# Kernel optimization log

Measured on AMD Instinct MI355X. Metric: run time of the kernel, lower is better.

The kernel has to match this reference:

```python
import jax, jax.numpy as jnp
import numpy as np
import itertools

# ---- constants matching init_kwargs ----
ED, KD, NH, AR = 512, 16, 8, 4
D = AR * KD            # 64 == ED // NH (required by cascade residual add)
DH = D * NH            # 512
RES, WS = 28, 7
SCALE = KD ** -0.5
KS = [7, 5, 3, 3, 3, 3, 3, 3]

# relative-position bias index map for a WSxWS window (49 unique |offset| pairs)
def _bias_idx(ws):
    pts = list(itertools.product(range(ws), range(ws)))
    offs, idxs = {}, []
    for p1 in pts:
        for p2 in pts:
            o = (abs(p1[0] - p2[0]), abs(p1[1] - p2[1]))
            if o not in offs:
                offs[o] = len(offs)
            idxs.append(offs[o])
    return np.array(idxs, dtype=np.int32).reshape(ws * ws, ws * ws), len(offs)
BIAS_IDX, N_OFFS = _bias_idx(WS)  # [49,49], 49


def dwconv(x, w, b):
    """Depthwise conv, stride 1, SAME padding (pad = k//2, odd k). w: [C,1,k,k]."""
    y = jax.lax.conv_general_dilated(x, w, (1, 1), 'SAME',
                                     dimension_numbers=('NCHW', 'OIHW', 'NCHW'),
                                     feature_group_count=x.shape[1])
    return y + b[None, :, None, None]


def pw(x, w, b):
    """1x1 conv (fused Conv2d_BN in eval mode). w: [O,C]."""
    return jnp.einsum('bchw,oc->bohw', x, w) + b[None, :, None, None]


def mlp(x, w1, b1, w2, b2):
    return pw(jax.nn.hard_swish(pw(x, w1, b1)), w2, b2)


def window_partition(x, ws):
    B, C, H, W = x.shape
    nH, nW = H // ws, W // ws
    return x.reshape(B, C, nH, ws, nW, ws).transpose(0, 2, 4, 1, 3, 5).reshape(B * nH * nW, C, ws, ws)


def window_merge(xw, B, H, W, ws):
    nH, nW = H // ws, W // ws
    C = xw.shape[1]
    return xw.reshape(B, nH, nW, C, ws, ws).transpose(0, 3, 1, 4, 2, 5).reshape(B, C, H, W)


def cascade_attention(xw, qkv_w, qkv_b, dwq_ws, dwq_bs, ab, proj_w, proj_b):
    """xw: [Bw, ED, WS, WS]; ab: [NH, N, N] bias table gathered per head."""
    Bw, C, H, W = xw.shape
    N = H * W
    spx = jnp.split(xw, NH, axis=1)          # NH chunks of [Bw, ED//NH, H, W]
    sp = spx[0]
    outs = []
    for i in range(NH):  # heads are structurally distinct (kernel sizes) -> Python loop ok
        if i > 0:
            sp = sp + spx[i]
        y = pw(sp, qkv_w[i], qkv_b[i])       # [Bw, 2*KD+D, H, W]
        q, k, v = jnp.split(y, [KD, 2 * KD], axis=1)
        q = dwconv(q, dwq_ws[i], dwq_bs[i])  # per-head depthwise conv on q
        qf = q.reshape(Bw, KD, N)
        kf = k.reshape(Bw, KD, N)
        vf = v.reshape(Bw, D, N)
        attn = jnp.einsum('bcn,bcm->bnm', qf, kf) * SCALE + ab[i]
        attn = jax.nn.softmax(attn, axis=-1)
        sp = jnp.einsum('bdm,bnm->bdn', vf, attn).reshape(Bw, D, H, W)
        outs.append(sp)
    y = jnp.concatenate(outs, axis=1)        # [Bw, DH, H, W]
    y = jax.nn.hard_swish(y)                 # proj = Sequential(act, Conv2d_BN)
    return pw(y, proj_w, proj_b)


def _forward(x, dw0_w, dw0_b, ffn0_w1, ffn0_b1, ffn0_w2, ffn0_b2,
             qkv_w, qkv_b, dwq_w7, dwq_b7, dwq_w5, dwq_b5, dwq_w3, dwq_b3,
             attn_bias, proj_w, proj_b,
             dw1_w, dw1_b, ffn1_w1, ffn1_b1, ffn1_w2, ffn1_b2):
    B, C, H, W = x.shape
    dwq_ws = [dwq_w7, dwq_w5] + [dwq_w3[i] for i in range(6)]
    dwq_bs = [dwq_b7, dwq_b5] + [dwq_b3[i] for i in range(6)]
    ab = attn_bias[:, BIAS_IDX]              # [NH, 49, 49]
    x = x + dwconv(x, dw0_w, dw0_b)
    x = x + mlp(x, ffn0_w1, ffn0_b1, ffn0_w2, ffn0_b2)
    xw = window_partition(x, WS)
    aw = cascade_attention(xw, qkv_w, qkv_b, dwq_ws, dwq_bs, ab, proj_w, proj_b)
    x = x + window_merge(aw, B, H, W, WS)
    x = x + dwconv(x, dw1_w, dw1_b)
    x = x + mlp(x, ffn1_w1, ffn1_b1, ffn1_w2, ffn1_b2)
    return x


def setup_inputs() -> dict:
    key = jax.random.key(0)
    ks = jax.random.split(key, 24)
    B = 64
    r = lambda k, shape, s=0.05: (jax.random.normal(k, shape, dtype=jnp.float32) * s)
    qkv_out = 2 * KD + D  # 96
    inp = {
        'x': jax.random.normal(ks[0], (B, ED, RES, RES), dtype=jnp.float32),
        'dw0_w': r(ks[1], (ED, 1, 3, 3)), 'dw0_b': r(ks[2], (ED,)),
        'ffn0_w1': r(ks[3], (2 * ED, ED)), 'ffn0_b1': r(ks[4], (2 * ED,)),
        'ffn0_w2': r(ks[5], (ED, 2 * ED)), 'ffn0_b2': r(ks[6], (ED,)),
        'qkv_w': r(ks[7], (NH, qkv_out, ED // NH)), 'qkv_b': r(ks[8], (NH, qkv_out)),
        'dwq_w7': r(ks[9], (KD, 1, 7, 7)), 'dwq_b7': r(ks[10], (KD,)),
        'dwq_w5': r(ks[11], (KD, 1, 5, 5)), 'dwq_b5': r(ks[12], (KD,)),
        'dwq_w3': r(ks[13], (6, KD, 1, 3, 3)), 'dwq_b3': r(ks[14], (6, KD)),
        'attn_bias': r(ks[15], (NH, N_OFFS)),
        'proj_w': r(ks[16], (ED, DH)), 'proj_b': r(ks[17], (ED,)),
        'dw1_w': r(ks[18], (ED, 1, 3, 3)), 'dw1_b': r(ks[19], (ED,)),
        'ffn1_w1': r(ks[20], (2 * ED, ED)), 'ffn1_b1': r(ks[21], (2 * ED,)),
        'ffn1_w2': r(ks[22], (ED, 2 * ED)), 'ffn1_b2': r(ks[23], (ED,)),
    }
    return inp


def reference(x, dw0_w, dw0_b, ffn0_w1, ffn0_b1, ffn0_w2, ffn0_b2,
              qkv_w, qkv_b, dwq_w7, dwq_b7, dwq_w5, dwq_b5, dwq_w3, dwq_b3,
              attn_bias, proj_w, proj_b,
              dw1_w, dw1_b, ffn1_w1, ffn1_b1, ffn1_w2, ffn1_b2):
    return _forward(x, dw0_w, dw0_b, ffn0_w1, ffn0_b1, ffn0_w2, ffn0_b2,
                    qkv_w, qkv_b, dwq_w7, dwq_b7, dwq_w5, dwq_b5, dwq_w3, dwq_b3,
                    attn_bias, proj_w, proj_b,
                    dw1_w, dw1_b, ffn1_w1, ffn1_b1, ffn1_w2, ffn1_b2)
```

## Files before the change

### kernel.cpp

```cpp
#include <hip/hip_runtime.h>
#include <hip/hip_bf16.h>


#define NPOS 50176
#define NEL ((size_t)512 * NPOS)

typedef __hip_bfloat16 hbf;
typedef unsigned int u32;
typedef __attribute__((ext_vector_type(8))) short short8;
typedef __attribute__((ext_vector_type(4))) short bf16x4;
typedef __attribute__((ext_vector_type(4))) float f32x4;

__device__ __forceinline__ float hswish(float v) {
    float t = fminf(fmaxf(v + 3.0f, 0.0f), 6.0f);
    return v * t * (1.0f / 6.0f);
}
__device__ __forceinline__ float b2f(hbf x) { return __bfloat162float(x); }
__device__ __forceinline__ hbf f2b(float x) { return __float2bfloat16(x); }

__device__ __forceinline__ unsigned short bfb(float v) {
    hbf h = f2b(v); unsigned short u; __builtin_memcpy(&u, &h, 2); return u;
}
__device__ __forceinline__ unsigned pk2(float a, float b) {
    return (unsigned)bfb(a) | ((unsigned)bfb(b) << 16);
}
__device__ __forceinline__ int swz128(int row, int b) {
    return row * 128 + (b ^ ((row & 7) << 4));
}
__device__ __forceinline__ void gl16(const hbf* g, short* l) {
    __builtin_amdgcn_global_load_lds((const __attribute__((address_space(1))) u32*)g,
                                     (__attribute__((address_space(3))) u32*)l,
                                     16, 0, 0);
}

__device__ __forceinline__ bool is_bf16_buf(const void* probe) {
    const unsigned* w = (const unsigned*)probe;
    int hits = 0;
#pragma unroll
    for (int i = 0; i < 64; i++) {
        unsigned lo = w[i] & 0xFFFFu;
        unsigned e = (lo >> 7) & 0xFFu;
        hits += ((e >= 100u && e <= 140u) || lo == 0u) ? 1 : 0;
    }
    return hits >= 32;
}

#define OFF_W01  0
#define OFF_W02  524288
#define OFF_W11  1048576
#define OFF_W12  1572864
#define OFF_PW   2097152
#define OFF_QKVW 2359296
#define OFF_QKVB 2408448
#define OFF_W7   2409216
#define OFF_B7   2410000
#define OFF_W5   2410016
#define OFF_B5   2410416
#define OFF_W3   2410432
#define OFF_B3   2411296
#define OFF_AB   2411392
#define OFF_D0W  2411784
#define OFF_D0B  2416392
#define OFF_D1W  2416904
#define OFF_D1B  2421512
#define OFF_B01  2422024
#define OFF_B02  2423048
#define OFF_B11  2423560
#define OFF_B12  2424584
#define OFF_PB   2425096
#define ARENA_TOT 2425608

struct CvtArgs { const void* src; int off; int count; };
struct CvtTable { CvtArgs t[23]; };

__global__ __launch_bounds__(256) void k_convert(CvtTable tab, hbf* __restrict__ arena,
                                                 const void* __restrict__ probe) {
    CvtArgs a = tab.t[blockIdx.y];
    int i = blockIdx.x * 256 + threadIdx.x;
    if (i >= a.count) return;
    bool isbf = is_bf16_buf(probe);
    float v = isbf ? b2f(((const hbf*)a.src)[i]) : ((const float*)a.src)[i];
    arena[a.off + i] = f2b(v);
}

template <int EPI, int K, int GX, bool SWAP>
__global__ __launch_bounds__(256) void k_gemm(const hbf* __restrict__ A,
                                              const hbf* __restrict__ B,
                                              const hbf* __restrict__ bias,
                                              const void* __restrict__ res,
                                              void* __restrict__ out,
                                              const void* __restrict__ probe) {
    __shared__ short sA[128 * 64];
    __shared__ short sB[128 * 64];

    const int tid = threadIdx.x;
    const int wave = tid >> 6, lane = tid & 63;
    const int col = lane & 15, quad = lane >> 4;

    const int lin = blockIdx.y * GX + blockIdx.x;
    const int q8 = (GX * (int)gridDim.y) >> 3;
    const int swz = (lin & 7) * q8 + (lin >> 3);
    const int bx = swz % GX, by = swz / GX;
    const int m0 = (SWAP ? by : bx) * 128, n0 = (SWAP ? bx : by) * 128;

    const int wm = (wave & 1) * 64, wn = (wave >> 1) * 64;

    const int rowl = lane >> 3;
    const int kswz = ((lane & 7) ^ rowl) * 8;
    const hbf* Ag = A + (size_t)(m0 + wave * 32 + rowl) * K + kswz;
    const hbf* Bg = B + (size_t)(n0 + wave * 32 + rowl) * K + kswz;
    short* sAw = sA + (wave * 32) * 64;
    short* sBw = sB + (wave * 32) * 64;

    f32x4 acc[4][4];
#pragma unroll
    for (int i = 0; i < 4; i++)
#pragma unroll
        for (int j = 0; j < 4; j++) acc[i][j] = (f32x4){0.f, 0.f, 0.f, 0.f};

    for (int k0 = 0; k0 < K; k0 += 64) {
        __syncthreads();
#pragma unroll
        for (int t = 0; t < 4; t++) {
            gl16(Ag + k0 + (size_t)t * 8 * K, sAw + t * 8 * 64);
            gl16(Bg + k0 + (size_t)t * 8 * K, sBw + t * 8 * 64);
        }
        __syncthreads();

#pragma unroll
        for (int kk = 0; kk < 2; kk++) {
            short8 af[4], bfr[4];
#pragma unroll
            for (int i = 0; i < 4; i++) {
                int r = wm + i * 16 + col;
                af[i] = *(const short8*)(sA + r * 64 + (((kk * 4 + quad) ^ (r & 7)) * 8));
            }
#pragma unroll
            for (int j = 0; j < 4; j++) {
                int r = wn + j * 16 + col;
                bfr[j] = *(const short8*)(sB + r * 64 + (((kk * 4 + quad) ^ (r & 7)) * 8));
            }
#pragma unroll
            for (int i = 0; i < 4; i++)
#pragma unroll
                for (int j = 0; j < 4; j++)
                    acc[i][j] = __builtin_amdgcn_mfma_f32_16x16x32_bf16(af[i], bfr[j], acc[i][j], 0, 0, 0);
        }
    }

    bool outbf = false;
    if constexpr (EPI == 3) outbf = is_bf16_buf(probe);

#pragma unroll
    for (int i = 0; i < 4; i++) {
#pragma unroll
        for (int j = 0; j < 4; j++) {
#pragma unroll
            for (int r = 0; r < 4; r++) {
                int mi = m0 + wm + i * 16 + quad * 4 + r;
                int nj = n0 + wn + j * 16 + col;
                float v = acc[i][j][r];
                if constexpr (EPI == 0) {
                    v = hswish(v + b2f(bias[nj]));
                    ((hbf*)out)[(size_t)mi * 1024 + nj] = f2b(v);
                } else if constexpr (EPI == 1) {
                    v += b2f(bias[mi]) + b2f(((const hbf*)res)[(size_t)nj * 512 + mi]);
                    ((float*)out)[(size_t)mi * NPOS + nj] = v;
                } else if constexpr (EPI == 2) {
                    int w = nj / 49, p = nj % 49;
                    int nct = (w >> 4) * 784 + (((w >> 2) & 3) * 7 + p / 7) * 28 + (w & 3) * 7 + p % 7;
                    size_t oi = (size_t)mi * NPOS + nct;
                    v += b2f(bias[mi]) + ((const float*)res)[oi];
                    ((float*)out)[oi] = v;
                } else {
                    int b = nj / 784, hw = nj % 784;
                    v += b2f(bias[mi]) + ((const float*)res)[(size_t)mi * NPOS + nj];
                    size_t oi = ((size_t)b * 512 + mi) * 784 + hw;
                    if (outbf) ((hbf*)out)[oi] = f2b(v);
                    else ((float*)out)[oi] = v;
                }
            }
        }
    }
}

template <int MODE, bool ISBF>
__device__ void dw_body(float* sIn, float* sW, const void* __restrict__ in,
                        const hbf* __restrict__ w, const hbf* __restrict__ bias,
                        hbf* __restrict__ outNK, float* __restrict__ outCT) {
    const int tid = threadIdx.x;
    const int tx = tid & 63, tg = tid >> 6;
    const int n0 = blockIdx.x * 64, c0 = blockIdx.y * 64;

    for (int e = tid; e < 640; e += 256) {
        int cc = e / 10, t = e - cc * 10;
        sW[e] = (t < 9) ? b2f(w[(c0 + cc) * 9 + t]) : b2f(bias[c0 + cc]);
    }

#pragma unroll
    for (int k = 0; k < 8; k++) {
        int idx = tid + k * 256;
        int ch = idx >> 5, j4 = idx & 31;
        int p = n0 - 32 + j4 * 4;
        p = p < 0 ? 0 : (p > NPOS - 4 ? NPOS - 4 : p);
        f32x4 v;
        if constexpr (MODE == 1) {
            v = *(const f32x4*)((const float*)in + (size_t)(c0 + ch) * NPOS + p);
        } else {
            int b = p / 784, hw = p - b * 784;
            size_t ix = ((size_t)b * 512 + c0 + ch) * 784 + hw;
            if constexpr (ISBF) {
                bf16x4 t4 = *(const bf16x4*)((const hbf*)in + ix);
#pragma unroll
                for (int j = 0; j < 4; j++) {
                    unsigned u = (unsigned)(unsigned short)t4[j] << 16;
                    v[j] = __uint_as_float(u);
                }
            } else {
                v = *(const f32x4*)((const float*)in + ix);
            }
        }
        *(f32x4*)(sIn + ch * 128 + j4 * 4) = v;
    }
    __syncthreads();

    const int n = n0 + tx;
    const int b = n / 784, hw = n - b * 784;
    const int r = hw / 28, s = hw - r * 28;
    const float mrow[3] = { r > 0 ? 1.f : 0.f, 1.f, r < 27 ? 1.f : 0.f };
    const float mcol[3] = { s > 0 ? 1.f : 0.f, 1.f, s < 27 ? 1.f : 0.f };

    float vals[16];
#pragma unroll
    for (int i = 0; i < 16; i++) {
        const int cc = tg + 4 * i;
        const float* row = sIn + cc * 128 + 32 + tx;
        float acc = sW[cc * 10 + 9];
        float center = row[0];
#pragma unroll
        for (int dy = 0; dy < 3; dy++)
#pragma unroll
            for (int dx = 0; dx < 3; dx++)
                acc = fmaf(row[(dy - 1) * 28 + (dx - 1)],
                           mrow[dy] * mcol[dx] * sW[cc * 10 + dy * 3 + dx], acc);
        float val = center + acc;
        vals[i] = val;
        if constexpr (MODE == 1) outCT[(size_t)(c0 + cc) * NPOS + n] = val;
    }
    __syncthreads();

    float (*tile)[65] = (float (*)[65])sIn;
#pragma unroll
    for (int i = 0; i < 16; i++) tile[tg + 4 * i][tx] = vals[i];
    __syncthreads();
    for (int q = tg; q < 64; q += 4)
        outNK[(size_t)(n0 + q) * 512 + c0 + tx] = f2b(tile[tx][q]);
}

template <int MODE>
__global__ __launch_bounds__(256, 4) void k_dw(const void* in, const hbf* w, const hbf* b,
                                               hbf* outNK, float* outCT, const void* probe) {
    __shared__ float sIn[64 * 128];
    __shared__ float sW[64 * 10];
    if constexpr (MODE == 1) {
        dw_body<1, false>(sIn, sW, in, w, b, outNK, outCT);
    } else {
        if (is_bf16_buf(probe)) dw_body<0, true>(sIn, sW, in, w, b, outNK, outCT);
        else dw_body<0, false>(sIn, sW, in, w, b, outNK, outCT);
    }
}

__global__ __launch_bounds__(256, 4) void k_attn(const float* __restrict__ y2,
                                                 const hbf* __restrict__ arena,
                                                 hbf* __restrict__ ywin) {
    __shared__ short spT[64 * 64];
    __shared__ short vbT[64 * 64];
    __shared__ short atb[64 * 64];
    __shared__ short qT[64 * 40];
    __shared__ short kT[64 * 40];
    __shared__ float qraw[16 * 52];
    __shared__ float abf[8 * 49];

    const int tid = threadIdx.x;
    const int wave = tid >> 6, lane = tid & 63;
    const int col = lane & 15, quad = lane >> 4;
    const int w = ((blockIdx.x & 7) << 7) | (blockIdx.x >> 3);
    const int wb = w >> 4, wh = (w >> 2) & 3, ww = w & 3;
    const size_t base = (size_t)wb * 784 + (wh * 7) * 28 + ww * 7;

    for (int e = tid; e < 64 * 64; e += 256) { vbT[e] = 0; atb[e] = 0; }
    for (int e = tid; e < 64 * 16; e += 256) {
        int n = e >> 4, c = 16 + (e & 15);
        qT[n * 40 + c] = 0; kT[n * 40 + c] = 0;
    }
    for (int e = tid; e < 8 * 49; e += 256) abf[e] = b2f(arena[OFF_AB + e]);

    for (int e = tid; e < 64 * 49; e += 256) {
        int c = e / 49, n = e - c * 49;
        float v = y2[(size_t)c * NPOS + base + (n / 7) * 28 + (n % 7)];
        *(hbf*)((char*)spT + swz128(n, 2 * c)) = f2b(v);
    }

    int nj[4], posj[4], m7[4], mm7[4];
    bool vj[4];
#pragma unroll
    for (int j = 0; j < 4; j++) {
        nj[j] = j * 16 + col;
        vj[j] = nj[j] < 49;
        int nc = vj[j] ? nj[j] : 48;
        m7[j] = nc / 7; mm7[j] = nc - m7[j] * 7;
        posj[j] = m7[j] * 28 + mm7[j];
    }
    const int nq = wave * 16 + quad * 4;

#pragma unroll 1
    for (int h = 0; h < 8; h++) {
        __syncthreads();

        const hbf* wq = arena + OFF_QKVW + h * 96 * 64;
        const int brow = wave * 16 + col;
        short8 sb0 = *(const short8*)((const char*)spT + swz128(brow, quad * 16));
        short8 sb1 = *(const short8*)((const char*)spT + swz128(brow, 64 + quad * 16));
        f32x4 yacc[6];
#pragma unroll
        for (int i = 0; i < 6; i++) {
            short8 a0 = *(const short8*)(wq + (i * 16 + col) * 64 + quad * 8);
            short8 a1 = *(const short8*)(wq + (i * 16 + col) * 64 + 32 + quad * 8);
            f32x4 z = (f32x4){0.f, 0.f, 0.f, 0.f};
            z = __builtin_amdgcn_mfma_f32_16x16x32_bf16(a0, sb0, z, 0, 0, 0);
            z = __builtin_amdgcn_mfma_f32_16x16x32_bf16(a1, sb1, z, 0, 0, 0);
            yacc[i] = z;
        }
        if (brow < 49) {
            const int n = brow;
#pragma unroll
            for (int i = 0; i < 6; i++) {
                float vv[4];
#pragma unroll
                for (int r = 0; r < 4; r++)
                    vv[r] = yacc[i][r] + b2f(arena[OFF_QKVB + h * 96 + i * 16 + quad * 4 + r]);
                if (i == 0) {
#pragma unroll
                    for (int r = 0; r < 4; r++) qraw[(quad * 4 + r) * 52 + n] = vv[r];
                } else if (i == 1) {
                    *(unsigned*)((char*)kT + n * 80 + 8 * quad)     = pk2(vv[0], vv[1]);
                    *(unsigned*)((char*)kT + n * 80 + 8 * quad + 4) = pk2(vv[2], vv[3]);
                } else {
#pragma unroll
                    for (int r = 0; r < 4; r++) {
                        int d = (i - 2) * 16 + quad * 4 + r;
                        *(hbf*)((char*)vbT + swz128(d, 2 * n)) = f2b(vv[r]);
                    }
                }
            }
        }
        __syncthreads();

        const hbf* cw; const hbf* cb; int ks;
        if (h == 0)      { cw = arena + OFF_W7; cb = arena + OFF_B7; ks = 7; }
        else if (h == 1) { cw = arena + OFF_W5; cb = arena + OFF_B5; ks = 5; }
        else             { cw = arena + OFF_W3 + (h - 2) * 144; cb = arena + OFF_B3 + (h - 2) * 16; ks = 3; }
        const int pad = ks >> 1;
        for (int e = tid; e < 784; e += 256) {
            int c = e / 49, n = e - c * 49;
            int r = n / 7, s = n - r * 7;
            float acc = b2f(cb[c]);
            for (int dy = 0; dy < ks; dy++) {
                int rr = r + dy - pad;
                if (rr < 0 || rr >= 7) continue;
                for (int dx = 0; dx < ks; dx++) {
                    int ss = s + dx - pad;
                    if (ss < 0 || ss >= 7) continue;
                    acc += b2f(cw[c * ks * ks + dy * ks + dx]) * qraw[c * 52 + rr * 7 + ss];
                }
            }
            *(hbf*)((char*)qT + n * 80 + 2 * c) = f2b(acc * 0.25f);
        }
        __syncthreads();

        short8 qa = *(const short8*)((const char*)qT + (wave * 16 + col) * 80 + quad * 16);
        f32x4 sat[4];
#pragma unroll
        for (int j = 0; j < 4; j++) {
            short8 kb = *(const short8*)((const char*)kT + (j * 16 + col) * 80 + quad * 16);
            f32x4 z = (f32x4){0.f, 0.f, 0.f, 0.f};
            sat[j] = __builtin_amdgcn_mfma_f32_16x16x32_bf16(qa, kb, z, 0, 0, 0);
        }
#pragma unroll
        for (int r = 0; r < 4; r++) {
            int n = nq + r;
            int ncl = n < 49 ? n : 48;
            int n7 = ncl / 7, nn7 = ncl - n7 * 7;
            float v0 = sat[0][r] + abf[h * 49 + abs(n7 - m7[0]) * 7 + abs(nn7 - mm7[0])];
            float v1 = sat[1][r] + abf[h * 49 + abs(n7 - m7[1]) * 7 + abs(nn7 - mm7[1])];
            float v2 = sat[2][r] + abf[h * 49 + abs(n7 - m7[2]) * 7 + abs(nn7 - mm7[2])];
            float v3 = (col == 0) ? sat[3][r] + abf[h * 49 + abs(n7 - m7[3]) * 7 + abs(nn7 - mm7[3])]
                                  : -1e30f;
            float mx = fmaxf(fmaxf(v0, v1), fmaxf(v2, v3));
#pragma unroll
            for (int s = 1; s < 16; s <<= 1) mx = fmaxf(mx, __shfl_xor(mx, s));
            float p0 = __expf(v0 - mx), p1 = __expf(v1 - mx), p2 = __expf(v2 - mx);
            float p3 = (col == 0) ? __expf(v3 - mx) : 0.f;
            float sm = p0 + p1 + p2 + p3;
#pragma unroll
            for (int s = 1; s < 16; s <<= 1) sm += __shfl_xor(sm, s);
            float inv = 1.0f / sm;
            *(hbf*)((char*)atb + swz128(n, 2 * col))        = f2b(p0 * inv);
            *(hbf*)((char*)atb + swz128(n, 2 * (16 + col))) = f2b(p1 * inv);
            *(hbf*)((char*)atb + swz128(n, 2 * (32 + col))) = f2b(p2 * inv);
            if (col == 0) *(hbf*)((char*)atb + swz128(n, 2 * 48)) = f2b(p3 * inv);
        }
        __syncthreads();

        short8 va0 = *(const short8*)((const char*)vbT + swz128(wave * 16 + col, quad * 16));
        short8 va1 = *(const short8*)((const char*)vbT + swz128(wave * 16 + col, 64 + quad * 16));
#pragma unroll
        for (int j = 0; j < 4; j++) {
            short8 pb0 = *(const short8*)((const char*)atb + swz128(nj[j], quad * 16));
            short8 pb1 = *(const short8*)((const char*)atb + swz128(nj[j], 64 + quad * 16));
            f32x4 o = (f32x4){0.f, 0.f, 0.f, 0.f};
            o = __builtin_amdgcn_mfma_f32_16x16x32_bf16(va0, pb0, o, 0, 0, 0);
            o = __builtin_amdgcn_mfma_f32_16x16x32_bf16(va1, pb1, o, 0, 0, 0);
            if (vj[j]) {
                size_t yo = ((size_t)w * 49 + nj[j]) * 512 + h * 64 + nq;
                *(unsigned*)(ywin + yo)     = pk2(hswish(o[0]), hswish(o[1]));
                *(unsigned*)(ywin + yo + 2) = pk2(hswish(o[2]), hswish(o[3]));
                if (h < 7) {
                    const float* ys = y2 + (size_t)((h + 1) * 64 + nq) * NPOS + base + posj[j];
                    unsigned s0 = pk2(o[0] + ys[0],
                                      o[1] + ys[(size_t)NPOS]);
                    unsigned s1 = pk2(o[2] + ys[2 * (size_t)NPOS],
                                      o[3] + ys[3 * (size_t)NPOS]);
                    *(unsigned*)((char*)spT + swz128(nj[j], 2 * nq))     = s0;
                    *(unsigned*)((char*)spT + swz128(nj[j], 2 * nq + 4)) = s1;
                }
            }
        }
    }
}


extern "C" void kernel_launch(void* const* d_in, const int* in_sizes, int n_in,
                              void* d_out, int out_size, void* d_ws, size_t ws_size,
                              hipStream_t stream) {
    const void* x = d_in[0];

    if (ws_size < NEL * 10 + (size_t)ARENA_TOT * 2) return;

    uint8_t* p = (uint8_t*)d_ws;
    hbf*   R0 = (hbf*)p;
    hbf*   R1 = (hbf*)(p + NEL * 2);
    float* R2 = (float*)(p + NEL * 6);
    hbf*   arena = (hbf*)(p + NEL * 10);

    hbf*   y1t  = R0;
    hbf*   hid  = R1;
    float* y2f  = R2;
    hbf*   ywin = R0;
    float* x3f  = (float*)R1;
    float* x4f  = R2;
    hbf*   x4t  = R0;
    hbf*   hid2 = R1;

    CvtTable tab = {{
        { d_in[3],  OFF_W01,  524288 },
        { d_in[5],  OFF_W02,  524288 },
        { d_in[20], OFF_W11,  524288 },
        { d_in[22], OFF_W12,  524288 },
        { d_in[16], OFF_PW,   262144 },
        { d_in[7],  OFF_QKVW, 49152 },
        { d_in[8],  OFF_QKVB, 768 },
        { d_in[9],  OFF_W7,   784 },
        { d_in[10], OFF_B7,   16 },
        { d_in[11], OFF_W5,   400 },
        { d_in[12], OFF_B5,   16 },
        { d_in[13], OFF_W3,   864 },
        { d_in[14], OFF_B3,   96 },
        { d_in[15], OFF_AB,   392 },
        { d_in[1],  OFF_D0W,  4608 },
        { d_in[2],  OFF_D0B,  512 },
        { d_in[18], OFF_D1W,  4608 },
        { d_in[19], OFF_D1B,  512 },
        { d_in[4],  OFF_B01,  1024 },
        { d_in[6],  OFF_B02,  512 },
        { d_in[21], OFF_B11,  1024 },
        { d_in[23], OFF_B12,  512 },
        { d_in[17], OFF_PB,   512 },
    }};

    dim3 blk(256);

    k_convert<<<dim3(2048, 23), blk, 0, stream>>>(tab, arena, x);
    k_dw<0><<<dim3(NPOS / 64, 8), blk, 0, stream>>>(x, arena + OFF_D0W, arena + OFF_D0B, y1t, nullptr, x);
    k_gemm<0, 512, 8, true><<<dim3(8, 392), blk, 0, stream>>>(y1t, arena + OFF_W01, arena + OFF_B01, nullptr, hid, x);
    k_gemm<1, 1024, 4, false><<<dim3(4, 392), blk, 0, stream>>>(arena + OFF_W02, hid, arena + OFF_B02, y1t, y2f, x);
    k_attn<<<1024, blk, 0, stream>>>(y2f, arena, ywin);
    k_gemm<2, 512, 4, false><<<dim3(4, 392), blk, 0, stream>>>(arena + OFF_PW, ywin, arena + OFF_PB, y2f, x3f, x);
    k_dw<1><<<dim3(NPOS / 64, 8), blk, 0, stream>>>(x3f, arena + OFF_D1W, arena + OFF_D1B, x4t, x4f, x);
    k_gemm<0, 512, 8, true><<<dim3(8, 392), blk, 0, stream>>>(x4t, arena + OFF_W11, arena + OFF_B11, nullptr, hid2, x);
    k_gemm<3, 1024, 4, false><<<dim3(4, 392), blk, 0, stream>>>(arena + OFF_W12, hid2, arena + OFF_B12, x4f, d_out, x);
}
```

Measured before the change: 1.029 ms.

## Process two attention windows per block in cascade attention kernel

The attention kernel now handles two windows per workgroup, with all shared-memory buffers doubled and every per-head stage looping over both windows. This halves the grid and the number of barriers per window, and lets the per-head QKV weight loads be reused across two windows. In exchange, LDS use roughly doubles and launch bounds drop to 2 blocks per CU, which reduces occupancy. With only 512 blocks on a 256-CU part, the change also gives fewer waves to hide latency.

```diff
diff --git a/kernel.cpp b/kernel.cpp
--- a/kernel.cpp
+++ b/kernel.cpp
@@ -270,36 +270,48 @@
     }
 }
 
-__global__ __launch_bounds__(256, 4) void k_attn(const float* __restrict__ y2,
+__global__ __launch_bounds__(256, 2) void k_attn(const float* __restrict__ y2,
                                                  const hbf* __restrict__ arena,
                                                  hbf* __restrict__ ywin) {
-    __shared__ short spT[64 * 64];
-    __shared__ short vbT[64 * 64];
-    __shared__ short atb[64 * 64];
-    __shared__ short qT[64 * 40];
-    __shared__ short kT[64 * 40];
-    __shared__ float qraw[16 * 52];
+    __shared__ short spT[2][64 * 64];
+    __shared__ short vbT[2][64 * 64];
+    __shared__ short atb[2][64 * 64];
+    __shared__ short qT[2][64 * 40];
+    __shared__ short kT[2][64 * 40];
+    __shared__ float qraw[2][16 * 52];
     __shared__ float abf[8 * 49];
 
     const int tid = threadIdx.x;
     const int wave = tid >> 6, lane = tid & 63;
     const int col = lane & 15, quad = lane >> 4;
-    const int w = ((blockIdx.x & 7) << 7) | (blockIdx.x >> 3);
-    const int wb = w >> 4, wh = (w >> 2) & 3, ww = w & 3;
-    const size_t base = (size_t)wb * 784 + (wh * 7) * 28 + ww * 7;
-
-    for (int e = tid; e < 64 * 64; e += 256) { vbT[e] = 0; atb[e] = 0; }
+    const int pb = blockIdx.x;
+    const int bb = ((pb & 7) << 6) | (pb >> 3);
+    int wgl[2]; size_t base[2];
+#pragma unroll
+    for (int wi = 0; wi < 2; wi++) {
+        int w = 2 * bb + wi;
+        wgl[wi] = w;
+        int wb = w >> 4, wh = (w >> 2) & 3, ww = w & 3;
+        base[wi] = (size_t)wb * 784 + (wh * 7) * 28 + ww * 7;
+    }
+
+    for (int e = tid; e < 64 * 64; e += 256) {
+        vbT[0][e] = 0; vbT[1][e] = 0; atb[0][e] = 0; atb[1][e] = 0;
+    }
     for (int e = tid; e < 64 * 16; e += 256) {
         int n = e >> 4, c = 16 + (e & 15);
-        qT[n * 40 + c] = 0; kT[n * 40 + c] = 0;
+        qT[0][n * 40 + c] = 0; qT[1][n * 40 + c] = 0;
+        kT[0][n * 40 + c] = 0; kT[1][n * 40 + c] = 0;
     }
     for (int e = tid; e < 8 * 49; e += 256) abf[e] = b2f(arena[OFF_AB + e]);
 
-    for (int e = tid; e < 64 * 49; e += 256) {
-        int c = e / 49, n = e - c * 49;
-        float v = y2[(size_t)c * NPOS + base + (n / 7) * 28 + (n % 7)];
-        *(hbf*)((char*)spT + swz128(n, 2 * c)) = f2b(v);
-    }
+#pragma unroll
+    for (int wi = 0; wi < 2; wi++)
+        for (int e = tid; e < 64 * 49; e += 256) {
+            int c = e / 49, n = e - c * 49;
+            float v = y2[(size_t)c * NPOS + base[wi] + (n / 7) * 28 + (n % 7)];
+            *(hbf*)((char*)spT[wi] + swz128(n, 2 * c)) = f2b(v);
+        }
 
     int nj[4], posj[4], m7[4], mm7[4];
     bool vj[4];
@@ -319,37 +331,40 @@
 
         const hbf* wq = arena + OFF_QKVW + h * 96 * 64;
         const int brow = wave * 16 + col;
-        short8 sb0 = *(const short8*)((const char*)spT + swz128(brow, quad * 16));
-        short8 sb1 = *(const short8*)((const char*)spT + swz128(brow, 64 + quad * 16));
-        f32x4 yacc[6];
-#pragma unroll
-        for (int i = 0; i < 6; i++) {
-            short8 a0 = *(const short8*)(wq + (i * 16 + col) * 64 + quad * 8);
-            short8 a1 = *(const short8*)(wq + (i * 16 + col) * 64 + 32 + quad * 8);
-            f32x4 z = (f32x4){0.f, 0.f, 0.f, 0.f};
-            z = __builtin_amdgcn_mfma_f32_16x16x32_bf16(a0, sb0, z, 0, 0, 0);
-            z = __builtin_amdgcn_mfma_f32_16x16x32_bf16(a1, sb1, z, 0, 0, 0);
-            yacc[i] = z;
-        }
-        if (brow < 49) {
-            const int n = brow;
+#pragma unroll
+        for (int wi = 0; wi < 2; wi++) {
+            short8 sb0 = *(const short8*)((const char*)spT[wi] + swz128(brow, quad * 16));
+            short8 sb1 = *(const short8*)((const char*)spT[wi] + swz128(brow, 64 + quad * 16));
+            f32x4 yacc[6];
 #pragma unroll
             for (int i = 0; i < 6; i++) {
-                float vv[4];
-#pragma unroll
-                for (int r = 0; r < 4; r++)
-                    vv[r] = yacc[i][r] + b2f(arena[OFF_QKVB + h * 96 + i * 16 + quad * 4 + r]);
-                if (i == 0) {
-#pragma unroll
-                    for (int r = 0; r < 4; r++) qraw[(quad * 4 + r) * 52 + n] = vv[r];
-                } else if (i == 1) {
-                    *(unsigned*)((char*)kT + n * 80 + 8 * quad)     = pk2(vv[0], vv[1]);
-                    *(unsigned*)((char*)kT + n * 80 + 8 * quad + 4) = pk2(vv[2], vv[3]);
-                } else {
-#pragma unroll
-                    for (int r = 0; r < 4; r++) {
-                        int d = (i - 2) * 16 + quad * 4 + r;
-                        *(hbf*)((char*)vbT + swz128(d, 2 * n)) = f2b(vv[r]);
+                short8 a0 = *(const short8*)(wq + (i * 16 + col) * 64 + quad * 8);
+                short8 a1 = *(const short8*)(wq + (i * 16 + col) * 64 + 32 + quad * 8);
+                f32x4 z = (f32x4){0.f, 0.f, 0.f, 0.f};
+                z = __builtin_amdgcn_mfma_f32_16x16x32_bf16(a0, sb0, z, 0, 0, 0);
+                z = __builtin_amdgcn_mfma_f32_16x16x32_bf16(a1, sb1, z, 0, 0, 0);
+                yacc[i] = z;
+            }
+            if (brow < 49) {
+                const int n = brow;
+#pragma unroll
+                for (int i = 0; i < 6; i++) {
+                    float vv[4];
+#pragma unroll
+                    for (int r = 0; r < 4; r++)
+                        vv[r] = yacc[i][r] + b2f(arena[OFF_QKVB + h * 96 + i * 16 + quad * 4 + r]);
+                    if (i == 0) {
+#pragma unroll
+                        for (int r = 0; r < 4; r++) qraw[wi][(quad * 4 + r) * 52 + n] = vv[r];
+                    } else if (i == 1) {
+                        *(unsigned*)((char*)kT[wi] + n * 80 + 8 * quad)     = pk2(vv[0], vv[1]);
+                        *(unsigned*)((char*)kT[wi] + n * 80 + 8 * quad + 4) = pk2(vv[2], vv[3]);
+                    } else {
+#pragma unroll
+                        for (int r = 0; r < 4; r++) {
+                            int d = (i - 2) * 16 + quad * 4 + r;
+                            *(hbf*)((char*)vbT[wi] + swz128(d, 2 * n)) = f2b(vv[r]);
+                        }
                     }
                 }
             }
@@ -361,78 +376,86 @@
         else if (h == 1) { cw = arena + OFF_W5; cb = arena + OFF_B5; ks = 5; }
         else             { cw = arena + OFF_W3 + (h - 2) * 144; cb = arena + OFF_B3 + (h - 2) * 16; ks = 3; }
         const int pad = ks >> 1;
-        for (int e = tid; e < 784; e += 256) {
-            int c = e / 49, n = e - c * 49;
-            int r = n / 7, s = n - r * 7;
-            float acc = b2f(cb[c]);
-            for (int dy = 0; dy < ks; dy++) {
-                int rr = r + dy - pad;
-                if (rr < 0 || rr >= 7) continue;
-                for (int dx = 0; dx < ks; dx++) {
-                    int ss = s + dx - pad;
-                    if (ss < 0 || ss >= 7) continue;
-                    acc += b2f(cw[c * ks * ks + dy * ks + dx]) * qraw[c * 52 + rr * 7 + ss];
+#pragma unroll
+        for (int wi = 0; wi < 2; wi++)
+            for (int e = tid; e < 784; e += 256) {
+                int c = e / 49, n = e - c * 49;
+                int r = n / 7, s = n - r * 7;
+                float acc = b2f(cb[c]);
+                for (int dy = 0; dy < ks; dy++) {
+                    int rr = r + dy - pad;
+                    if (rr < 0 || rr >= 7) continue;
+                    for (int dx = 0; dx < ks; dx++) {
+                        int ss = s + dx - pad;
+                        if (ss < 0 || ss >= 7) continue;
+                        acc += b2f(cw[c * ks * ks + dy * ks + dx]) * qraw[wi][c * 52 + rr * 7 + ss];
+                    }
                 }
-            }
-            *(hbf*)((char*)qT + n * 80 + 2 * c) = f2b(acc * 0.25f);
-        }
+                *(hbf*)((char*)qT[wi] + n * 80 + 2 * c) = f2b(acc * 0.25f);
+            }
         __syncthreads();
 
-        short8 qa = *(const short8*)((const char*)qT + (wave * 16 + col) * 80 + quad * 16);
-        f32x4 sat[4];
-#pragma unroll
-        for (int j = 0; j < 4; j++) {
-            short8 kb = *(const short8*)((const char*)kT + (j * 16 + col) * 80 + quad * 16);
-            f32x4 z = (f32x4){0.f, 0.f, 0.f, 0.f};
-            sat[j] = __builtin_amdgcn_mfma_f32_16x16x32_bf16(qa, kb, z, 0, 0, 0);
-        }
-#pragma unroll
-        for (int r = 0; r < 4; r++) {
-            int n = nq + r;
-            int ncl = n < 49 ? n : 48;
-            int n7 = ncl / 7, nn7 = ncl - n7 * 7;
-            float v0 = sat[0][r] + abf[h * 49 + abs(n7 - m7[0]) * 7 + abs(nn7 - mm7[0])];
-            float v1 = sat[1][r] + abf[h * 49 + abs(n7 - m7[1]) * 7 + abs(nn7 - mm7[1])];
-            float v2 = sat[2][r] + abf[h * 49 + abs(n7 - m7[2]) * 7 + abs(nn7 - mm7[2])];
-            float v3 = (col == 0) ? sat[3][r] + abf[h * 49 + abs(n7 - m7[3]) * 7 + abs(nn7 - mm7[3])]
-                                  : -1e30f;
-            float mx = fmaxf(fmaxf(v0, v1), fmaxf(v2, v3));
-#pragma unroll
-            for (int s = 1; s < 16; s <<= 1) mx = fmaxf(mx, __shfl_xor(mx, s));
-            float p0 = __expf(v0 - mx), p1 = __expf(v1 - mx), p2 = __expf(v2 - mx);
-            float p3 = (col == 0) ? __expf(v3 - mx) : 0.f;
-            float sm = p0 + p1 + p2 + p3;
-#pragma unroll
-            for (int s = 1; s < 16; s <<= 1) sm += __shfl_xor(sm, s);
-            float inv = 1.0f / sm;
-            *(hbf*)((char*)atb + swz128(n, 2 * col))        = f2b(p0 * inv);
-            *(hbf*)((char*)atb + swz128(n, 2 * (16 + col))) = f2b(p1 * inv);
-            *(hbf*)((char*)atb + swz128(n, 2 * (32 + col))) = f2b(p2 * inv);
-            if (col == 0) *(hbf*)((char*)atb + swz128(n, 2 * 48)) = f2b(p3 * inv);
+#pragma unroll
+        for (int wi = 0; wi < 2; wi++) {
+            short8 qa = *(const short8*)((const char*)qT[wi] + (wave * 16 + col) * 80 + quad * 16);
+            f32x4 sat[4];
+#pragma unroll
+            for (int j = 0; j < 4; j++) {
+                short8 kb = *(const short8*)((const char*)kT[wi] + (j * 16 + col) * 80 + quad * 16);
+                f32x4 z = (f32x4){0.f, 0.f, 0.f, 0.f};
+                sat[j] = __builtin_amdgcn_mfma_f32_16x16x32_bf16(qa, kb, z, 0, 0, 0);
+            }
+#pragma unroll
+            for (int r = 0; r < 4; r++) {
+                int n = nq + r;
+                int ncl = n < 49 ? n : 48;
+                int n7 = ncl / 7, nn7 = ncl - n7 * 7;
+                float v0 = sat[0][r] + abf[h * 49 + abs(n7 - m7[0]) * 7 + abs(nn7 - mm7[0])];
+                float v1 = sat[1][r] + abf[h * 49 + abs(n7 - m7[1]) * 7 + abs(nn7 - mm7[1])];
+                float v2 = sat[2][r] + abf[h * 49 + abs(n7 - m7[2]) * 7 + abs(nn7 - mm7[2])];
+                float v3 = (col == 0) ? sat[3][r] + abf[h * 49 + abs(n7 - m7[3]) * 7 + abs(nn7 - mm7[3])]
+                                      : -1e30f;
+                float mx = fmaxf(fmaxf(v0, v1), fmaxf(v2, v3));
+#pragma unroll
+                for (int s = 1; s < 16; s <<= 1) mx = fmaxf(mx, __shfl_xor(mx, s));
+                float p0 = __expf(v0 - mx), p1 = __expf(v1 - mx), p2 = __expf(v2 - mx);
+                float p3 = (col == 0) ? __expf(v3 - mx) : 0.f;
+                float sm = p0 + p1 + p2 + p3;
+#pragma unroll
+                for (int s = 1; s < 16; s <<= 1) sm += __shfl_xor(sm, s);
+                float inv = 1.0f / sm;
+                *(hbf*)((char*)atb[wi] + swz128(n, 2 * col))        = f2b(p0 * inv);
+                *(hbf*)((char*)atb[wi] + swz128(n, 2 * (16 + col))) = f2b(p1 * inv);
+                *(hbf*)((char*)atb[wi] + swz128(n, 2 * (32 + col))) = f2b(p2 * inv);
+                if (col == 0) *(hbf*)((char*)atb[wi] + swz128(n, 2 * 48)) = f2b(p3 * inv);
+            }
         }
         __syncthreads();
 
-        short8 va0 = *(const short8*)((const char*)vbT + swz128(wave * 16 + col, quad * 16));
-        short8 va1 = *(const short8*)((const char*)vbT + swz128(wave * 16 + col, 64 + quad * 16));
-#pragma unroll
-        for (int j = 0; j < 4; j++) {
-            short8 pb0 = *(const short8*)((const char*)atb + swz128(nj[j], quad * 16));
-            short8 pb1 = *(const short8*)((const char*)atb + swz128(nj[j], 64 + quad * 16));
-            f32x4 o = (f32x4){0.f, 0.f, 0.f, 0.f};
-            o = __builtin_amdgcn_mfma_f32_16x16x32_bf16(va0, pb0, o, 0, 0, 0);
-            o = __builtin_amdgcn_mfma_f32_16x16x32_bf16(va1, pb1, o, 0, 0, 0);
-            if (vj[j]) {
-                size_t yo = ((size_t)w * 49 + nj[j]) * 512 + h * 64 + nq;
-                *(unsigned*)(ywin + yo)     = pk2(hswish(o[0]), hswish(o[1]));
-                *(unsigned*)(ywin + yo + 2) = pk2(hswish(o[2]), hswish(o[3]));
-                if (h < 7) {
-                    const float* ys = y2 + (size_t)((h + 1) * 64 + nq) * NPOS + base + posj[j];
-                    unsigned s0 = pk2(o[0] + ys[0],
-                                      o[1] + ys[(size_t)NPOS]);
-                    unsigned s1 = pk2(o[2] + ys[2 * (size_t)NPOS],
-                                      o[3] + ys[3 * (size_t)NPOS]);
-                    *(unsigned*)((char*)spT + swz128(nj[j], 2 * nq))     = s0;
-                    *(unsigned*)((char*)spT + swz128(nj[j], 2 * nq + 4)) = s1;
+#pragma unroll
+        for (int wi = 0; wi < 2; wi++) {
+            short8 va0 = *(const short8*)((const char*)vbT[wi] + swz128(wave * 16 + col, quad * 16));
+            short8 va1 = *(const short8*)((const char*)vbT[wi] + swz128(wave * 16 + col, 64 + quad * 16));
+#pragma unroll
+            for (int j = 0; j < 4; j++) {
+                short8 pb0 = *(const short8*)((const char*)atb[wi] + swz128(nj[j], quad * 16));
+                short8 pb1 = *(const short8*)((const char*)atb[wi] + swz128(nj[j], 64 + quad * 16));
+                f32x4 o = (f32x4){0.f, 0.f, 0.f, 0.f};
+                o = __builtin_amdgcn_mfma_f32_16x16x32_bf16(va0, pb0, o, 0, 0, 0);
+                o = __builtin_amdgcn_mfma_f32_16x16x32_bf16(va1, pb1, o, 0, 0, 0);
+                if (vj[j]) {
+                    size_t yo = ((size_t)wgl[wi] * 49 + nj[j]) * 512 + h * 64 + nq;
+                    *(unsigned*)(ywin + yo)     = pk2(hswish(o[0]), hswish(o[1]));
+                    *(unsigned*)(ywin + yo + 2) = pk2(hswish(o[2]), hswish(o[3]));
+                    if (h < 7) {
+                        const float* ys = y2 + (size_t)((h + 1) * 64 + nq) * NPOS + base[wi] + posj[j];
+                        unsigned s0 = pk2(o[0] + ys[0],
+                                          o[1] + ys[(size_t)NPOS]);
+                        unsigned s1 = pk2(o[2] + ys[2 * (size_t)NPOS],
+                                          o[3] + ys[3 * (size_t)NPOS]);
+                        *(unsigned*)((char*)spT[wi] + swz128(nj[j], 2 * nq))     = s0;
+                        *(unsigned*)((char*)spT[wi] + swz128(nj[j], 2 * nq + 4)) = s1;
+                    }
                 }
             }
         }
@@ -494,7 +517,7 @@
     k_dw<0><<<dim3(NPOS / 64, 8), blk, 0, stream>>>(x, arena + OFF_D0W, arena + OFF_D0B, y1t, nullptr, x);
     k_gemm<0, 512, 8, true><<<dim3(8, 392), blk, 0, stream>>>(y1t, arena + OFF_W01, arena + OFF_B01, nullptr, hid, x);
     k_gemm<1, 1024, 4, false><<<dim3(4, 392), blk, 0, stream>>>(arena + OFF_W02, hid, arena + OFF_B02, y1t, y2f, x);
-    k_attn<<<1024, blk, 0, stream>>>(y2f, arena, ywin);
+    k_attn<<<512, blk, 0, stream>>>(y2f, arena, ywin);
     k_gemm<2, 512, 4, false><<<dim3(4, 392), blk, 0, stream>>>(arena + OFF_PW, ywin, arena + OFF_PB, y2f, x3f, x);
     k_dw<1><<<dim3(NPOS / 64, 8), blk, 0, stream>>>(x3f, arena + OFF_D1W, arena + OFF_D1B, x4t, x4f, x);
     k_gemm<0, 512, 8, true><<<dim3(8, 392), blk, 0, stream>>>(x4t, arena + OFF_W11, arena + OFF_B11, nullptr, hid2, x);
```

New measurement: 1.058 ms. 2.8% more time.
